# Optimization experiments

Hardware: AMD Instinct MI355X
Metric: run time of the kernel (lower is better)

The kernel has to match this reference:

```python
import jax, jax.numpy as jnp
import numpy as np
from functools import partial

L, H, DH, D, DFF, S, NCLS = 12, 16, 32, 512, 2048, 17, 10
PATCH_DIM = 192  # 3*8*8


def layernorm(x, s, b, eps=1e-5):
    m = jnp.mean(x, axis=-1, keepdims=True)
    v = jnp.var(x, axis=-1, keepdims=True)
    return (x - m) * jax.lax.rsqrt(v + eps) * s + b


def setup_inputs() -> dict:
    key = jax.random.key(0)
    ks = iter(jax.random.split(key, 32))
    w = lambda *shape: jax.random.normal(next(ks), shape, dtype=jnp.float32) * 0.02
    d = {
        'x': jax.random.normal(next(ks), (2048, 3, 32, 32), dtype=jnp.float32),
        'conv_w': w(3, 3, 16, 16),              # OIHW
        'conv_b': jnp.zeros((3,), jnp.float32),
        'h_w1': w(PATCH_DIM, D), 'h_b1': jnp.zeros((D,), jnp.float32),
        'h_w2': w(D, D), 'h_b2': jnp.zeros((D,), jnp.float32),
        'cls_tok': w(1, D),
        'pos_emb': w(S, D),
        # stacked per-layer params, leading dim L
        'ln1_s': jnp.ones((L, D), jnp.float32), 'ln1_b': jnp.zeros((L, D), jnp.float32),
        'qkv_w': w(L, D, 3 * D), 'qkv_b': jnp.zeros((L, 3 * D), jnp.float32),
        'proj_w': w(L, D, D), 'proj_b': jnp.zeros((L, D), jnp.float32),
        'ln2_s': jnp.ones((L, D), jnp.float32), 'ln2_b': jnp.zeros((L, D), jnp.float32),
        'mlp_w1': w(L, D, DFF), 'mlp_b1': jnp.zeros((L, DFF), jnp.float32),
        'mlp_w2': w(L, DFF, D), 'mlp_b2': jnp.zeros((L, D), jnp.float32),
        'fin_s': jnp.ones((D,), jnp.float32), 'fin_b': jnp.zeros((D,), jnp.float32),
        'cls_w': w(D, NCLS), 'cls_b': jnp.zeros((NCLS,), jnp.float32),
    }
    return d


def _encoder_step(h, p):
    B = h.shape[0]
    n = layernorm(h, p['ln1_s'], p['ln1_b'])
    qkv = n @ p['qkv_w'] + p['qkv_b']                      # (B,S,3D)
    qkv = qkv.reshape(B, S, 3, H, DH).transpose(2, 0, 3, 1, 4)  # (3,B,H,S,DH)
    q, k, v = qkv[0], qkv[1], qkv[2]
    scores = jnp.einsum('bhsd,bhtd->bhst', q, k) / np.sqrt(DH).astype(np.float32)
    attn = jax.nn.softmax(scores, axis=-1)
    o = jnp.einsum('bhst,bhtd->bhsd', attn, v)
    o = o.transpose(0, 2, 1, 3).reshape(B, S, D)
    h = h + o @ p['proj_w'] + p['proj_b']
    n2 = layernorm(h, p['ln2_s'], p['ln2_b'])
    mlp = jax.nn.gelu(n2 @ p['mlp_w1'] + p['mlp_b1'], approximate=False) @ p['mlp_w2'] + p['mlp_b2']
    return h + mlp, None


def reference(x, conv_w, conv_b, h_w1, h_b1, h_w2, h_b2, cls_tok, pos_emb,
              ln1_s, ln1_b, qkv_w, qkv_b, proj_w, proj_b,
              ln2_s, ln2_b, mlp_w1, mlp_b1, mlp_w2, mlp_b2,
              fin_s, fin_b, cls_w, cls_b):
    B = x.shape[0]
    # conv, torch 'same' for k=16: pad (7,8)
    xc = jax.lax.conv_general_dilated(x, conv_w, (1, 1), [(7, 8), (7, 8)],
                                      dimension_numbers=('NCHW', 'OIHW', 'NCHW'))
    xc = xc + conv_b[None, :, None, None]
    # patchify: b c (h p1) (w p2) -> b (h w) (c p1 p2)
    p = xc.reshape(B, 3, 4, 8, 4, 8).transpose(0, 2, 4, 1, 3, 5).reshape(B, 16, PATCH_DIM)
    hid = p @ h_w1 + h_b1
    hid = jnp.where(hid > 0, hid, 0.1 * hid)  # LeakyReLU(0.1)
    hid = hid @ h_w2 + h_b2
    # cls token appended at END (as in original)
    hid = jnp.concatenate([hid, jnp.broadcast_to(cls_tok[None], (B, 1, D))], axis=1)
    h = hid + pos_emb[None]
    layer_params = {'ln1_s': ln1_s, 'ln1_b': ln1_b, 'qkv_w': qkv_w, 'qkv_b': qkv_b,
                    'proj_w': proj_w, 'proj_b': proj_b, 'ln2_s': ln2_s, 'ln2_b': ln2_b,
                    'mlp_w1': mlp_w1, 'mlp_b1': mlp_b1, 'mlp_w2': mlp_w2, 'mlp_b2': mlp_b2}
    h, _ = jax.lax.scan(_encoder_step, h, layer_params)
    h = layernorm(h, fin_s, fin_b)
    cls = h[:, 0, :]  # original reads index 0 (a patch token)
    return cls @ cls_w + cls_b
```

## Files before the change

### kernel.cpp

```cpp
#include <hip/hip_runtime.h>
#include <stdint.h>

#define NB   2048
#define SEQ  17
#define DIM  512
#define NTOK (NB * SEQ)
#define NPAT (NB * 16)

typedef __bf16 v8bf __attribute__((ext_vector_type(8)));
typedef float  f32x4 __attribute__((ext_vector_type(4)));

typedef const __attribute__((address_space(1))) void GVoid;
typedef __attribute__((address_space(3))) void LVoid;

__device__ __forceinline__ uint16_t f2bf(float f) {
  uint32_t u = __float_as_uint(f);
  uint32_t r = u + 0x7FFFu + ((u >> 16) & 1u);
  return (uint16_t)(r >> 16);
}
__device__ __forceinline__ float bf2f(uint16_t h) {
  return __uint_as_float(((uint32_t)h) << 16);
}
__device__ __forceinline__ void load16_lds(const void* g, void* l) {
  __builtin_amdgcn_global_load_lds((GVoid*)g, (LVoid*)l, 16, 0, 0);
}

__global__ __launch_bounds__(256) void transpose_cast(
    const float* __restrict__ in, uint16_t* __restrict__ out, int K, int N,
    size_t in_ls, size_t out_ls) {
  const float* src = in + (size_t)blockIdx.z * in_ls;
  uint16_t* dst = out + (size_t)blockIdx.z * out_ls;
  __shared__ uint16_t t[64][65];
  int k0 = blockIdx.y * 64, n0 = blockIdx.x * 64;
  int tid = threadIdx.x;
  int c = tid & 63, r0 = tid >> 6;
#pragma unroll
  for (int i = 0; i < 16; i++) {
    int r = i * 4 + r0;
    t[c][r] = f2bf(src[(size_t)(k0 + r) * N + n0 + c]);
  }
  __syncthreads();
#pragma unroll
  for (int i = 0; i < 16; i++) {
    int rn = i * 4 + r0;
    dst[(size_t)(n0 + rn) * K + k0 + c] = t[rn][c];
  }
}

__global__ __launch_bounds__(256) void xpad_fill(
    const float* __restrict__ x, uint16_t* __restrict__ xp) {
  int idx = blockIdx.x * 256 + threadIdx.x;
  int c8 = idx % 6;
  int r = (idx / 6) % 48;
  int i = (idx / 288) % 3;
  int b = idx / 864;
  int col0 = c8 * 8;
  uint16_t v[8];
  const float* src = x + ((size_t)(b * 3 + i) * 32 + (r - 7)) * 32;
#pragma unroll
  for (int e = 0; e < 8; e++) {
    int col = col0 + e;
    float val = (r >= 7 && r < 39 && col >= 7 && col < 39) ? src[col - 7] : 0.f;
    v[e] = f2bf(val);
  }
  *(uint4*)&xp[(((size_t)b * 3 + i) * 48 + r) * 48 + col0] = *(const uint4*)v;
}

__global__ __launch_bounds__(256) void build_G(
    const float* __restrict__ w, uint16_t* __restrict__ G) {
  int idx = blockIdx.x * 256 + threadIdx.x;
  if (idx >= 1792 * 192) return;
  int j = idx % 192, k = idx / 192;
  int o = j >> 6, ry = (j >> 3) & 7, rx = j & 7;
  int i = k / 576, rem = k - i * 576;
  int dy = rem / 24, dx = rem % 24;
  float val = 0.f;
  if (i < 3) {
    int ky = dy - ry, kx = dx - rx;
    if (ky >= 0 && ky < 16 && kx >= 0 && kx < 16)
      val = w[o * 768 + i * 256 + ky * 16 + kx];
  }
  G[idx] = f2bf(val);
}

__global__ __launch_bounds__(256) void bias_eff_kernel(
    const float* __restrict__ h_b1, const float* __restrict__ cb,
    const uint16_t* __restrict__ h1w, float* __restrict__ be) {
  int d = blockIdx.x * 256 + threadIdx.x;
  if (d >= 512) return;
  float s = h_b1[d];
#pragma unroll
  for (int o = 0; o < 3; o++) {
    float so = 0.f;
    for (int j = 0; j < 64; j++) so += bf2f(h1w[(size_t)d * 192 + o * 64 + j]);
    s += cb[o] * so;
  }
  be[d] = s;
}

template <int EPI, int ASRC>
__global__ __launch_bounds__(256, 4) void gemm128(
    const uint16_t* __restrict__ A, const uint16_t* __restrict__ W,
    const float* __restrict__ bias, uint16_t* __restrict__ outb,
    float* __restrict__ outf, const float* __restrict__ pos,
    int M, int N, int K, int lda, int ldw, int ldo) {
  __shared__ uint16_t As[128 * 64];
  __shared__ uint16_t Bs[128 * 64];
  const int tid = threadIdx.x;
  const int w = tid >> 6, l = tid & 63;
  const int lr = l & 15, lk = l >> 4;
  const int wm = w >> 1, wn = w & 1;

  int flat = blockIdx.y * gridDim.x + blockIdx.x;
  int nwg = gridDim.x * gridDim.y;
  int q = nwg >> 3, r = nwg & 7;
  int xcd = flat & 7, idx = flat >> 3;
  int f2 = (xcd < r ? xcd * (q + 1) : r * (q + 1) + (xcd - r) * q) + idx;
  const int m0 = (f2 / gridDim.x) * 128, n0 = (f2 % gridDim.x) * 128;

  f32x4 acc[4][4];
#pragma unroll
  for (int i = 0; i < 4; i++)
#pragma unroll
    for (int j = 0; j < 4; j++) acc[i][j] = (f32x4){0.f, 0.f, 0.f, 0.f};

  const int gr8 = l >> 3;
  const int csw = ((l & 7) ^ gr8) * 8;

  size_t abase[4];
  if (ASRC == 1) {
#pragma unroll
    for (int i = 0; i < 4; i++) {
      int rr = m0 + w * 32 + i * 8 + gr8;
      int b = rr >> 4, patch = rr & 15;
      int py = patch >> 2, px = patch & 3;
      abase[i] = (size_t)b * 6912 + py * 384 + px * 8;
    }
  }

  const int nkt = K >> 6;
  for (int kt = 0; kt < nkt; kt++) {
    const uint16_t* Bb = W + (size_t)n0 * ldw + (size_t)kt * 64;
    if (ASRC == 0) {
      const uint16_t* Ab = A + (size_t)m0 * lda + (size_t)kt * 64;
#pragma unroll
      for (int i = 0; i < 4; i++) {
        load16_lds(Ab + (size_t)(w * 32 + i * 8 + gr8) * lda + csw, As + w * 2048 + i * 512);
        load16_lds(Bb + (size_t)(w * 32 + i * 8 + gr8) * ldw + csw, Bs + w * 2048 + i * 512);
      }
    } else {
      int c8 = kt * 8 + ((l & 7) ^ gr8);
      int ii = c8 / 72, rem = c8 - ii * 72;
      int dy = rem / 3, dx0 = (rem - dy * 3) * 8;
      size_t koff = (size_t)ii * 2304 + dy * 48 + dx0;
#pragma unroll
      for (int i = 0; i < 4; i++) {
        load16_lds(A + abase[i] + koff, As + w * 2048 + i * 512);
        load16_lds(Bb + (size_t)(w * 32 + i * 8 + gr8) * ldw + csw, Bs + w * 2048 + i * 512);
      }
    }
    __syncthreads();
    {
      const int xm = lr & 7;
#pragma unroll
      for (int kk = 0; kk < 64; kk += 32) {
        const int j = (kk >> 3) + lk;
        const int pc = (j ^ xm) << 3;
        v8bf a[4], b[4];
#pragma unroll
        for (int mi = 0; mi < 4; mi++)
          a[mi] = *(const v8bf*)&As[(wm * 64 + mi * 16 + lr) * 64 + pc];
#pragma unroll
        for (int ni = 0; ni < 4; ni++)
          b[ni] = *(const v8bf*)&Bs[(wn * 64 + ni * 16 + lr) * 64 + pc];
#pragma unroll
        for (int mi = 0; mi < 4; mi++)
#pragma unroll
          for (int ni = 0; ni < 4; ni++)
            acc[mi][ni] = __builtin_amdgcn_mfma_f32_16x16x32_bf16(a[mi], b[ni], acc[mi][ni], 0, 0, 0);
      }
    }
    __syncthreads();
  }

#pragma unroll
  for (int mi = 0; mi < 4; mi++) {
#pragma unroll
    for (int ni = 0; ni < 4; ni++) {
      int col = n0 + wn * 64 + ni * 16 + lr;
      float bv = bias ? bias[col] : 0.f;
#pragma unroll
      for (int q2 = 0; q2 < 4; q2++) {
        int row = m0 + wm * 64 + mi * 16 + lk * 4 + q2;
        float v = acc[mi][ni][q2] + bv;
        if (EPI == 0) {
          outb[(size_t)row * ldo + col] = f2bf(v);
        } else if (EPI == 1) {
          v = v > 0.f ? v : 0.1f * v;
          outb[(size_t)row * ldo + col] = f2bf(v);
        } else if (EPI == 2) {
          float u = 1.5957691216057308f * (v + 0.044715f * v * v * v);
          v = v / (1.f + __expf(-u));
          outb[(size_t)row * ldo + col] = f2bf(v);
        } else if (EPI == 3) {
          size_t o = (size_t)row * ldo + col;
          outb[o] = f2bf(bf2f(outb[o]) + v);
        } else {
          int bb = row >> 4, ss = row & 15;
          outb[((size_t)bb * 17 + ss) * 512 + col] = f2bf(v + pos[ss * 512 + col]);
        }
      }
    }
  }
}

__global__ __launch_bounds__(256) void ln_kernel(
    const uint16_t* __restrict__ h, const float* __restrict__ s,
    const float* __restrict__ b, uint16_t* __restrict__ out) {
  int wid = threadIdx.x >> 6, l = threadIdx.x & 63;
  int row = blockIdx.x * 4 + wid;
  uint4 u = *(const uint4*)(h + (size_t)row * 512 + l * 8);
  const uint16_t* pu = (const uint16_t*)&u;
  float v[8];
#pragma unroll
  for (int i = 0; i < 8; i++) v[i] = bf2f(pu[i]);
  float sum = 0.f, sq = 0.f;
#pragma unroll
  for (int i = 0; i < 8; i++) { sum += v[i]; sq += v[i] * v[i]; }
#pragma unroll
  for (int off = 1; off < 64; off <<= 1) {
    sum += __shfl_xor(sum, off);
    sq += __shfl_xor(sq, off);
  }
  float mean = sum * (1.f / 512.f);
  float var = sq * (1.f / 512.f) - mean * mean;
  float rs = rsqrtf(var + 1e-5f);
  float4 s0 = *(const float4*)(s + l * 8);
  float4 s1 = *(const float4*)(s + l * 8 + 4);
  float4 b0 = *(const float4*)(b + l * 8);
  float4 b1 = *(const float4*)(b + l * 8 + 4);
  float sv[8] = {s0.x, s0.y, s0.z, s0.w, s1.x, s1.y, s1.z, s1.w};
  float bv[8] = {b0.x, b0.y, b0.z, b0.w, b1.x, b1.y, b1.z, b1.w};
  uint16_t pk[8];
#pragma unroll
  for (int i = 0; i < 8; i++) pk[i] = f2bf((v[i] - mean) * rs * sv[i] + bv[i]);
  *(uint4*)(out + (size_t)row * 512 + l * 8) = *(const uint4*)pk;
}

__global__ __launch_bounds__(64) void attn_kernel(
    const uint16_t* __restrict__ qkv, uint16_t* __restrict__ o) {
  int bh = blockIdx.x;
  int b = bh >> 4, h = bh & 15;
  __shared__ float Q[17][33], Kk[17][33], V[17][33], P[17][18];
  int tid = threadIdx.x;
  const uint16_t* base = qkv + (size_t)b * SEQ * 1536 + h * 32;
  for (int idx = tid; idx < 204; idx += 64) {
    int mat = idx / 68, rem = idx % 68;
    int s = rem >> 2, c = rem & 3;
    uint4 u = *(const uint4*)(base + (size_t)s * 1536 + mat * 512 + c * 8);
    const uint16_t* pu = (const uint16_t*)&u;
    float* dst = (mat == 0 ? Q[s] : mat == 1 ? Kk[s] : V[s]) + c * 8;
#pragma unroll
    for (int e = 0; e < 8; e++) dst[e] = bf2f(pu[e]);
  }
  __syncthreads();
  for (int idx = tid; idx < 289; idx += 64) {
    int i = idx / 17, j = idx % 17;
    float acc = 0.f;
#pragma unroll
    for (int d = 0; d < 32; d++) acc += Q[i][d] * Kk[j][d];
    P[i][j] = acc * 0.17677669529663687f;
  }
  __syncthreads();
  if (tid < 17) {
    float m = -1e30f;
    for (int j = 0; j < 17; j++) m = fmaxf(m, P[tid][j]);
    float sum = 0.f;
    for (int j = 0; j < 17; j++) { float e = __expf(P[tid][j] - m); P[tid][j] = e; sum += e; }
    float inv = 1.f / sum;
    for (int j = 0; j < 17; j++) P[tid][j] *= inv;
  }
  __syncthreads();
  uint16_t* ob = o + (size_t)b * SEQ * 512 + h * 32;
  for (int idx = tid; idx < 68; idx += 64) {
    int s = idx >> 2, c = idx & 3;
    float acc[8] = {0, 0, 0, 0, 0, 0, 0, 0};
#pragma unroll
    for (int t = 0; t < 17; t++) {
      float p = P[s][t];
      const float* vr = &V[t][c * 8];
#pragma unroll
      for (int e = 0; e < 8; e++) acc[e] += p * vr[e];
    }
    uint16_t pk[8];
#pragma unroll
    for (int e = 0; e < 8; e++) pk[e] = f2bf(acc[e]);
    *(uint4*)(ob + (size_t)s * 512 + c * 8) = *(const uint4*)pk;
  }
}

__global__ void fill_cls(const float* __restrict__ cls_tok,
                         const float* __restrict__ pos, uint16_t* __restrict__ h) {
  int b = blockIdx.x, d = threadIdx.x;
  h[((size_t)b * SEQ + 16) * 512 + d] = f2bf(cls_tok[d] + pos[16 * 512 + d]);
}

__global__ __launch_bounds__(64) void final_head(
    const uint16_t* __restrict__ h, const float* __restrict__ fs,
    const float* __restrict__ fb, const float* __restrict__ cw,
    const float* __restrict__ cb, float* __restrict__ out) {
  int b = blockIdx.x;
  const uint16_t* x = h + (size_t)b * SEQ * 512;
  int l = threadIdx.x;
  uint4 u = *(const uint4*)(x + l * 8);
  const uint16_t* pu = (const uint16_t*)&u;
  float v[8];
  float sum = 0.f, sq = 0.f;
#pragma unroll
  for (int i = 0; i < 8; i++) { v[i] = bf2f(pu[i]); sum += v[i]; sq += v[i] * v[i]; }
#pragma unroll
  for (int off = 1; off < 64; off <<= 1) { sum += __shfl_xor(sum, off); sq += __shfl_xor(sq, off); }
  float mean = sum * (1.f / 512.f);
  float var = sq * (1.f / 512.f) - mean * mean;
  float rs = rsqrtf(var + 1e-5f);
  __shared__ float n[512];
#pragma unroll
  for (int i = 0; i < 8; i++) n[l * 8 + i] = (v[i] - mean) * rs * fs[l * 8 + i] + fb[l * 8 + i];
  __syncthreads();
  if (l < 10) {
    float acc = cb[l];
    for (int d = 0; d < 512; d++) acc += n[d] * cw[d * 10 + l];
    out[(size_t)b * 10 + l] = acc;
  }
}

extern "C" void kernel_launch(void* const* d_in, const int* in_sizes, int n_in,
                              void* d_out, int out_size, void* d_ws, size_t ws_size,
                              hipStream_t stream) {
  const float* x       = (const float*)d_in[0];
  const float* conv_w  = (const float*)d_in[1];
  const float* conv_b  = (const float*)d_in[2];
  const float* h_w1    = (const float*)d_in[3];
  const float* h_b1    = (const float*)d_in[4];
  const float* h_w2    = (const float*)d_in[5];
  const float* h_b2    = (const float*)d_in[6];
  const float* cls_tok = (const float*)d_in[7];
  const float* pos_emb = (const float*)d_in[8];
  const float* ln1_s   = (const float*)d_in[9];
  const float* ln1_b   = (const float*)d_in[10];
  const float* qkv_w   = (const float*)d_in[11];
  const float* qkv_b   = (const float*)d_in[12];
  const float* proj_w  = (const float*)d_in[13];
  const float* proj_b  = (const float*)d_in[14];
  const float* ln2_s   = (const float*)d_in[15];
  const float* ln2_b   = (const float*)d_in[16];
  const float* mlp_w1  = (const float*)d_in[17];
  const float* mlp_b1  = (const float*)d_in[18];
  const float* mlp_w2  = (const float*)d_in[19];
  const float* mlp_b2  = (const float*)d_in[20];
  const float* fin_s   = (const float*)d_in[21];
  const float* fin_b   = (const float*)d_in[22];
  const float* cls_w   = (const float*)d_in[23];
  const float* cls_b   = (const float*)d_in[24];

  size_t off = 0;
  char* wsb = (char*)d_ws;
  auto take = [&](size_t bytes) -> void* {
    void* p = wsb + off;
    off += (bytes + 255) & ~(size_t)255;
    return p;
  };
  uint16_t* h1w  = (uint16_t*)take((size_t)512 * 192 * 2);
  uint16_t* h2w  = (uint16_t*)take((size_t)512 * 512 * 2);
  uint16_t* h    = (uint16_t*)take((size_t)NTOK * 512 * 2);
  uint16_t* nbuf = (uint16_t*)take((size_t)NTOK * 512 * 2);
  uint16_t* big  = (uint16_t*)take((size_t)NTOK * 2048 * 2);
  if (off > ws_size) return;
  size_t base_end = off;

  uint16_t* wqA = (uint16_t*)take((size_t)12 * 1536 * 512 * 2);
  uint16_t* wpA = (uint16_t*)take((size_t)12 * 512 * 512 * 2);
  uint16_t* w1A = (uint16_t*)take((size_t)12 * 2048 * 512 * 2);
  uint16_t* w2A = (uint16_t*)take((size_t)12 * 512 * 2048 * 2);
  bool all_fit = (off <= ws_size);
  uint16_t *wq = wqA, *wp = wpA, *w1 = w1A, *w2 = w2A;
  if (!all_fit) {
    off = base_end;
    wq = (uint16_t*)take((size_t)1536 * 512 * 2);
    wp = (uint16_t*)take((size_t)512 * 512 * 2);
    w1 = (uint16_t*)take((size_t)2048 * 512 * 2);
    w2 = (uint16_t*)take((size_t)512 * 2048 * 2);
    if (off > ws_size) return;
  }

  uint16_t* xpad = big;
  uint16_t* G    = (uint16_t*)((char*)big + 28311552);
  uint16_t* weff = (uint16_t*)((char*)big + 28311552 + 688128);
  float*    beff = (float*)((char*)big + 28311552 + 688128 + 1835008);
  uint16_t* hid1 = nbuf;

  dim3 blk(256);
  transpose_cast<<<dim3(8, 3), blk, 0, stream>>>(h_w1, h1w, 192, 512, 0, 0);
  transpose_cast<<<dim3(8, 8), blk, 0, stream>>>(h_w2, h2w, 512, 512, 0, 0);
  if (all_fit) {
    transpose_cast<<<dim3(24, 8, 12), blk, 0, stream>>>(qkv_w, wqA, 512, 1536,
                                                        (size_t)512 * 1536, (size_t)1536 * 512);
    transpose_cast<<<dim3(8, 8, 12), blk, 0, stream>>>(proj_w, wpA, 512, 512,
                                                       (size_t)512 * 512, (size_t)512 * 512);
    transpose_cast<<<dim3(32, 8, 12), blk, 0, stream>>>(mlp_w1, w1A, 512, 2048,
                                                        (size_t)512 * 2048, (size_t)2048 * 512);
    transpose_cast<<<dim3(8, 32, 12), blk, 0, stream>>>(mlp_w2, w2A, 2048, 512,
                                                        (size_t)2048 * 512, (size_t)512 * 2048);
  }

  xpad_fill<<<dim3(NB * 3 * 48 * 6 / 256), blk, 0, stream>>>(x, xpad);
  build_G<<<dim3((1792 * 192 + 255) / 256), blk, 0, stream>>>(conv_w, G);
  bias_eff_kernel<<<dim3(2), blk, 0, stream>>>(h_b1, conv_b, h1w, beff);
  gemm128<0, 0><<<dim3(14, 4), blk, 0, stream>>>(h1w, G, nullptr, weff, nullptr, nullptr,
                                                 512, 1792, 192, 192, 192, 1792);
  gemm128<1, 1><<<dim3(4, 256), blk, 0, stream>>>(xpad, weff, beff, hid1, nullptr, nullptr,
                                                  NPAT, 512, 1728, 0, 1792, 512);
  gemm128<4, 0><<<dim3(4, 256), blk, 0, stream>>>(hid1, h2w, h_b2, h, nullptr, pos_emb,
                                                  NPAT, 512, 512, 512, 512, 512);
  fill_cls<<<dim3(NB), dim3(512), 0, stream>>>(cls_tok, pos_emb, h);

  for (int l = 0; l < 12; l++) {
    uint16_t *wq_l, *wp_l, *w1_l, *w2_l;
    if (all_fit) {
      wq_l = wqA + (size_t)l * 1536 * 512;
      wp_l = wpA + (size_t)l * 512 * 512;
      w1_l = w1A + (size_t)l * 2048 * 512;
      w2_l = w2A + (size_t)l * 512 * 2048;
    } else {
      wq_l = wq; wp_l = wp; w1_l = w1; w2_l = w2;
      transpose_cast<<<dim3(24, 8), blk, 0, stream>>>(qkv_w + (size_t)l * 512 * 1536, wq, 512, 1536, 0, 0);
      transpose_cast<<<dim3(8, 8), blk, 0, stream>>>(proj_w + (size_t)l * 512 * 512, wp, 512, 512, 0, 0);
      transpose_cast<<<dim3(32, 8), blk, 0, stream>>>(mlp_w1 + (size_t)l * 512 * 2048, w1, 512, 2048, 0, 0);
      transpose_cast<<<dim3(8, 32), blk, 0, stream>>>(mlp_w2 + (size_t)l * 2048 * 512, w2, 2048, 512, 0, 0);
    }

    ln_kernel<<<dim3(NTOK / 4), blk, 0, stream>>>(h, ln1_s + l * 512, ln1_b + l * 512, nbuf);
    gemm128<0, 0><<<dim3(12, 272), blk, 0, stream>>>(nbuf, wq_l, qkv_b + l * 1536,
                                                     big, nullptr, nullptr,
                                                     NTOK, 1536, 512, 512, 512, 1536);
    attn_kernel<<<dim3(NB * 16), dim3(64), 0, stream>>>(big, nbuf);
    gemm128<3, 0><<<dim3(4, 272), blk, 0, stream>>>(nbuf, wp_l, proj_b + l * 512,
                                                    h, nullptr, nullptr,
                                                    NTOK, 512, 512, 512, 512, 512);
    ln_kernel<<<dim3(NTOK / 4), blk, 0, stream>>>(h, ln2_s + l * 512, ln2_b + l * 512, nbuf);
    gemm128<2, 0><<<dim3(16, 272), blk, 0, stream>>>(nbuf, w1_l, mlp_b1 + l * 2048,
                                                     big, nullptr, nullptr,
                                                     NTOK, 2048, 512, 512, 512, 2048);
    gemm128<3, 0><<<dim3(4, 272), blk, 0, stream>>>(big, w2_l, mlp_b2 + l * 512,
                                                    h, nullptr, nullptr,
                                                    NTOK, 512, 2048, 2048, 2048, 512);
  }
  final_head<<<dim3(NB), dim3(64), 0, stream>>>(h, fin_s, fin_b, cls_w, cls_b, (float*)d_out);
}
```

Baseline: 5.496 ms.

## Add 128x256-tile 512-thread GEMM with XCD-aware block remap for QKV and MLP1

Adds a new GEMM kernel with 8 waves and a 128x256 output tile, used for the QKV and first MLP projections in place of the 128x128 kernel. Each block loads its A tile once for twice as many output columns, which cuts redundant A traffic. Blocks are also remapped so that consecutive tiles land on the same XCD, improving L2 locality. The kernel is single-buffered, and the larger LDS footprint and 512-thread blocks may reduce occupancy.

```diff
diff --git a/kernel.cpp b/kernel.cpp
--- a/kernel.cpp
+++ b/kernel.cpp
@@ -23,6 +23,27 @@
 }
 __device__ __forceinline__ void load16_lds(const void* g, void* l) {
   __builtin_amdgcn_global_load_lds((GVoid*)g, (LVoid*)l, 16, 0, 0);
+}
+
+template <int EPI>
+__device__ __forceinline__ void epi_store(
+    float v, int row, int col, uint16_t* outb, const float* pos, int ldo) {
+  if (EPI == 0) {
+    outb[(size_t)row * ldo + col] = f2bf(v);
+  } else if (EPI == 1) {
+    v = v > 0.f ? v : 0.1f * v;
+    outb[(size_t)row * ldo + col] = f2bf(v);
+  } else if (EPI == 2) {
+    float u = 1.5957691216057308f * (v + 0.044715f * v * v * v);
+    v = v / (1.f + __expf(-u));
+    outb[(size_t)row * ldo + col] = f2bf(v);
+  } else if (EPI == 3) {
+    size_t o = (size_t)row * ldo + col;
+    outb[o] = f2bf(bf2f(outb[o]) + v);
+  } else {
+    int bb = row >> 4, ss = row & 15;
+    outb[((size_t)bb * 17 + ss) * 512 + col] = f2bf(v + pos[ss * 512 + col]);
+  }
 }
 
 __global__ __launch_bounds__(256) void transpose_cast(
@@ -192,23 +213,85 @@
 #pragma unroll
       for (int q2 = 0; q2 < 4; q2++) {
         int row = m0 + wm * 64 + mi * 16 + lk * 4 + q2;
-        float v = acc[mi][ni][q2] + bv;
-        if (EPI == 0) {
-          outb[(size_t)row * ldo + col] = f2bf(v);
-        } else if (EPI == 1) {
-          v = v > 0.f ? v : 0.1f * v;
-          outb[(size_t)row * ldo + col] = f2bf(v);
-        } else if (EPI == 2) {
-          float u = 1.5957691216057308f * (v + 0.044715f * v * v * v);
-          v = v / (1.f + __expf(-u));
-          outb[(size_t)row * ldo + col] = f2bf(v);
-        } else if (EPI == 3) {
-          size_t o = (size_t)row * ldo + col;
-          outb[o] = f2bf(bf2f(outb[o]) + v);
-        } else {
-          int bb = row >> 4, ss = row & 15;
-          outb[((size_t)bb * 17 + ss) * 512 + col] = f2bf(v + pos[ss * 512 + col]);
-        }
+        epi_store<EPI>(acc[mi][ni][q2] + bv, row, col, outb, pos, ldo);
+      }
+    }
+  }
+}
+
+template <int EPI>
+__global__ __launch_bounds__(512, 4) void gemmw(
+    const uint16_t* __restrict__ A, const uint16_t* __restrict__ W,
+    const float* __restrict__ bias, uint16_t* __restrict__ outb,
+    const float* __restrict__ pos,
+    int M, int N, int K, int lda, int ldw, int ldo) {
+  __shared__ uint16_t As[128 * 64];
+  __shared__ uint16_t Bs[256 * 64];
+  const int tid = threadIdx.x;
+  const int w = tid >> 6, l = tid & 63;
+  const int lr = l & 15, lk = l >> 4;
+  const int wm = w >> 2, wn = w & 3;
+
+  int flat = blockIdx.y * gridDim.x + blockIdx.x;
+  int nwg = gridDim.x * gridDim.y;
+  int q = nwg >> 3, r = nwg & 7;
+  int xcd = flat & 7, idx = flat >> 3;
+  int f2 = (xcd < r ? xcd * (q + 1) : r * (q + 1) + (xcd - r) * q) + idx;
+  const int m0 = (f2 / gridDim.x) * 128, n0 = (f2 % gridDim.x) * 256;
+
+  f32x4 acc[4][4];
+#pragma unroll
+  for (int i = 0; i < 4; i++)
+#pragma unroll
+    for (int j = 0; j < 4; j++) acc[i][j] = (f32x4){0.f, 0.f, 0.f, 0.f};
+
+  const int gr8 = l >> 3;
+  const int csw = ((l & 7) ^ gr8) * 8;
+
+  const int nkt = K >> 6;
+  for (int kt = 0; kt < nkt; kt++) {
+    const uint16_t* Ab = A + (size_t)m0 * lda + (size_t)kt * 64;
+    const uint16_t* Bb = W + (size_t)n0 * ldw + (size_t)kt * 64;
+#pragma unroll
+    for (int i = 0; i < 2; i++)
+      load16_lds(Ab + (size_t)(w * 16 + i * 8 + gr8) * lda + csw, As + w * 1024 + i * 512);
+#pragma unroll
+    for (int i = 0; i < 4; i++)
+      load16_lds(Bb + (size_t)(w * 32 + i * 8 + gr8) * ldw + csw, Bs + w * 2048 + i * 512);
+    __syncthreads();
+    {
+      const int xm = lr & 7;
+#pragma unroll
+      for (int kk = 0; kk < 64; kk += 32) {
+        const int j = (kk >> 3) + lk;
+        const int pc = (j ^ xm) << 3;
+        v8bf a[4], b[4];
+#pragma unroll
+        for (int mi = 0; mi < 4; mi++)
+          a[mi] = *(const v8bf*)&As[(wm * 64 + mi * 16 + lr) * 64 + pc];
+#pragma unroll
+        for (int ni = 0; ni < 4; ni++)
+          b[ni] = *(const v8bf*)&Bs[(wn * 64 + ni * 16 + lr) * 64 + pc];
+#pragma unroll
+        for (int mi = 0; mi < 4; mi++)
+#pragma unroll
+          for (int ni = 0; ni < 4; ni++)
+            acc[mi][ni] = __builtin_amdgcn_mfma_f32_16x16x32_bf16(a[mi], b[ni], acc[mi][ni], 0, 0, 0);
+      }
+    }
+    __syncthreads();
+  }
+
+#pragma unroll
+  for (int mi = 0; mi < 4; mi++) {
+#pragma unroll
+    for (int ni = 0; ni < 4; ni++) {
+      int col = n0 + wn * 64 + ni * 16 + lr;
+      float bv = bias ? bias[col] : 0.f;
+#pragma unroll
+      for (int q2 = 0; q2 < 4; q2++) {
+        int row = m0 + wm * 64 + mi * 16 + lk * 4 + q2;
+        epi_store<EPI>(acc[mi][ni][q2] + bv, row, col, outb, pos, ldo);
       }
     }
   }
@@ -399,7 +482,7 @@
   float*    beff = (float*)((char*)big + 28311552 + 688128 + 1835008);
   uint16_t* hid1 = nbuf;
 
-  dim3 blk(256);
+  dim3 blk(256), blkw(512);
   transpose_cast<<<dim3(8, 3), blk, 0, stream>>>(h_w1, h1w, 192, 512, 0, 0);
   transpose_cast<<<dim3(8, 8), blk, 0, stream>>>(h_w2, h2w, 512, 512, 0, 0);
   if (all_fit) {
@@ -440,17 +523,17 @@
     }
 
     ln_kernel<<<dim3(NTOK / 4), blk, 0, stream>>>(h, ln1_s + l * 512, ln1_b + l * 512, nbuf);
-    gemm128<0, 0><<<dim3(12, 272), blk, 0, stream>>>(nbuf, wq_l, qkv_b + l * 1536,
-                                                     big, nullptr, nullptr,
-                                                     NTOK, 1536, 512, 512, 512, 1536);
+    gemmw<0><<<dim3(6, 272), blkw, 0, stream>>>(nbuf, wq_l, qkv_b + l * 1536,
+                                                big, nullptr,
+                                                NTOK, 1536, 512, 512, 512, 1536);
     attn_kernel<<<dim3(NB * 16), dim3(64), 0, stream>>>(big, nbuf);
     gemm128<3, 0><<<dim3(4, 272), blk, 0, stream>>>(nbuf, wp_l, proj_b + l * 512,
                                                     h, nullptr, nullptr,
                                                     NTOK, 512, 512, 512, 512, 512);
     ln_kernel<<<dim3(NTOK / 4), blk, 0, stream>>>(h, ln2_s + l * 512, ln2_b + l * 512, nbuf);
-    gemm128<2, 0><<<dim3(16, 272), blk, 0, stream>>>(nbuf, w1_l, mlp_b1 + l * 2048,
-                                                     big, nullptr, nullptr,
-                                                     NTOK, 2048, 512, 512, 512, 2048);
+    gemmw<2><<<dim3(8, 272), blkw, 0, stream>>>(nbuf, w1_l, mlp_b1 + l * 2048,
+                                                big, nullptr,
+                                                NTOK, 2048, 512, 512, 512, 2048);
     gemm128<3, 0><<<dim3(4, 272), blk, 0, stream>>>(big, w2_l, mlp_b2 + l * 512,
                                                     h, nullptr, nullptr,
                                                     NTOK, 512, 2048, 2048, 2048, 512);
```

Result: slower. 5.639 ms (+2.6%).
